# Optimization experiments

Measured on AMD Instinct MI355X. Metric: run time of the kernel, lower is better.

Reference implementation:

```python
import jax, jax.numpy as jnp
import numpy as np

HEADS = 8
DIM_HEAD = 64
SCALE = DIM_HEAD ** -0.5  # q scaling
EPS = 1e-5  # channel LayerNorm eps (float32)


def setup_inputs() -> dict:
    key = jax.random.key(0)
    ks = jax.random.split(key, 4)
    B, C, H, W = 8, 256, 64, 64
    hd = HEADS * DIM_HEAD  # 512
    x = jax.random.normal(ks[0], (B, C, H, W), dtype=jnp.float32)
    w_qkv = jax.random.normal(ks[1], (3 * hd, C), dtype=jnp.float32) * 0.02  # 1x1 conv, no bias
    w_out = jax.random.normal(ks[2], (C, hd), dtype=jnp.float32) * 0.02     # 1x1 conv
    b_out = jax.random.normal(ks[3], (C,), dtype=jnp.float32) * 0.02
    g_ln = jnp.ones((C,), dtype=jnp.float32)  # LayerNorm gamma
    return {"x": x, "w_qkv": w_qkv, "w_out": w_out, "b_out": b_out, "g_ln": g_ln}


def reference(x, w_qkv, w_out, b_out, g_ln):
    B, C, H, W = x.shape
    n = H * W
    hd = HEADS * DIM_HEAD
    # 1x1 conv == per-pixel matmul: [B,C,H,W] x [3hd,C] -> [B,3hd,H,W]
    qkv = jnp.einsum('bchw,oc->bohw', x, w_qkv).reshape(B, 3, HEADS, DIM_HEAD, n)
    q, k, v = qkv[:, 0], qkv[:, 1], qkv[:, 2]  # each [B,h,d,n]
    q = jax.nn.softmax(q, axis=-2) * SCALE      # softmax over head-dim d
    k = jax.nn.softmax(k, axis=-1)              # softmax over spatial n
    v = v / n
    context = jnp.einsum('bhdn,bhen->bhde', k, v)   # [B,h,d,e]
    out = jnp.einsum('bhde,bhdn->bhen', context, q)  # [B,h,e,n]
    out = out.reshape(B, hd, H, W)
    # to_out: 1x1 conv + bias, then channel-wise LayerNorm (gamma only)
    y = jnp.einsum('bchw,oc->bohw', out, w_out) + b_out[None, :, None, None]
    mean = jnp.mean(y, axis=1, keepdims=True)
    var = jnp.var(y, axis=1, keepdims=True)  # unbiased=False
    return (y - mean) * jax.lax.rsqrt(var + EPS) * g_ln[None, :, None, None]
```

## Files before the change

### kernel.cpp

```cpp
#include <hip/hip_runtime.h>
#include <stdint.h>


#define NB    8
#define CCH   256
#define NSP   4096
#define O3    1536
#define NH    8
#define DH    64
#define CSTR  136

typedef unsigned short u16;
typedef unsigned int   u32;
typedef __bf16 bf16;
typedef bf16  bf16x8 __attribute__((ext_vector_type(8)));
typedef float f32x4  __attribute__((ext_vector_type(4)));
typedef u16   u16x8  __attribute__((ext_vector_type(8)));
typedef u16   u16x4  __attribute__((ext_vector_type(4)));

__device__ __forceinline__ float b2f(u16 h) {
  union { u32 u; float f; } x; x.u = ((u32)h) << 16; return x.f;
}
__device__ __forceinline__ u16 f2b(float f) {
  union { float f; u32 u; } x; x.f = f;
  u32 r = x.u + 0x7fffu + ((x.u >> 16) & 1u);
  return (u16)(r >> 16);
}
__device__ __forceinline__ int detect_bf(const void* g) {
  return ((const u32*)g)[0] != 0x3F800000u;
}
__device__ __forceinline__ void ldg2lds16(const u16* g, u16* l) {
  __builtin_amdgcn_global_load_lds((const __attribute__((address_space(1))) void*)g,
                                   (__attribute__((address_space(3))) void*)l,
                                   16, 0, 0);
}

#define TSTR 68
__global__ __launch_bounds__(256) void k_prep(const void* __restrict__ xv,
                                              const void* __restrict__ wv,
                                              u16* __restrict__ xT,
                                              u16* __restrict__ Wb,
                                              float* __restrict__ S,
                                              const void* __restrict__ g_lnv) {
  const int isbf = detect_bf(g_lnv);
  const int t = threadIdx.x;
  if (blockIdx.z == 8) {
    const int tid = blockIdx.y * 64 + blockIdx.x;
    if (tid < 192) {
      const int idx = tid * 256 + t;
      const int row = idx >> 5, cu = idx & 31;
      int didx;
      if (row < 512) {
        const int h = row >> 6, i = (row >> 4) & 3, fr = row & 15;
        const int ks = cu >> 2, quad = cu & 3;
        didx = ((h * 8 + ks) * 4 + i) * 64 + quad * 16 + fr;
      } else if (row < 1024) {
        didx = (512 + ((row - 512) >> 6) * 128 + (row & 63)) * 32 + cu;
      } else {
        didx = (512 + ((row - 1024) >> 6) * 128 + 64 + (row & 63)) * 32 + cu;
      }
      if (isbf) {
        reinterpret_cast<uint4*>(Wb)[didx] = reinterpret_cast<const uint4*>(wv)[idx];
      } else {
        float4 a = reinterpret_cast<const float4*>(wv)[idx * 2];
        float4 b = reinterpret_cast<const float4*>(wv)[idx * 2 + 1];
        ushort4 o0, o1;
        o0.x = f2b(a.x); o0.y = f2b(a.y); o0.z = f2b(a.z); o0.w = f2b(a.w);
        o1.x = f2b(b.x); o1.y = f2b(b.y); o1.z = f2b(b.z); o1.w = f2b(b.w);
        reinterpret_cast<ushort4*>(Wb)[didx * 2]     = o0;
        reinterpret_cast<ushort4*>(Wb)[didx * 2 + 1] = o1;
      }
    } else if (tid < 200) {
      reinterpret_cast<float2*>(S)[(tid - 192) * 256 + t] = (float2){0.f, 0.f};
    }
    return;
  }
  const int b = blockIdx.z, cb = blockIdx.y * 64, nb = blockIdx.x * 64;
  __shared__ u16 tile[64 * TSTR];
  if (isbf) {
    const u16* xb = (const u16*)xv;
#pragma unroll
    for (int rr = 0; rr < 2; ++rr) {
      const int u = t + 256 * rr;
      const int c = u >> 3, ch = u & 7;
      u16x8 v = *reinterpret_cast<const u16x8*>(
          xb + ((size_t)(b * CCH + cb + c) * NSP + nb + ch * 8));
      u16* dst = tile + c * TSTR + ch * 8;
      *reinterpret_cast<u16x4*>(dst)     = (u16x4){v[0], v[1], v[2], v[3]};
      *reinterpret_cast<u16x4*>(dst + 4) = (u16x4){v[4], v[5], v[6], v[7]};
    }
  } else {
    const float* xb = (const float*)xv;
#pragma unroll
    for (int rr = 0; rr < 4; ++rr) {
      const int u = t + 256 * rr;
      const int c = u >> 4, c4 = u & 15;
      float4 f = *reinterpret_cast<const float4*>(
          xb + ((size_t)(b * CCH + cb + c) * NSP + nb + c4 * 4));
      u16x4 o; o[0] = f2b(f.x); o[1] = f2b(f.y); o[2] = f2b(f.z); o[3] = f2b(f.w);
      *reinterpret_cast<u16x4*>(tile + c * TSTR + c4 * 4) = o;
    }
  }
  __syncthreads();
#pragma unroll
  for (int rr = 0; rr < 2; ++rr) {
    const int u = t + 256 * rr;
    const int n = u >> 3, cc = u & 7;
    u16x8 o;
#pragma unroll
    for (int e = 0; e < 8; ++e) o[e] = tile[(cc * 8 + e) * TSTR + n];
    *reinterpret_cast<u16x8*>(
        xT + ((size_t)(b * NSP + nb + n) * CCH + cb + cc * 8)) = o;
  }
}

__global__ __launch_bounds__(256) void k_kv_mfma(const u16* __restrict__ Wb,
                                                 const u16* __restrict__ xT,
                                                 float* __restrict__ S,
                                                 float* __restrict__ ctxp) {
  __shared__ __align__(16) u16 gbuf[16384];
  __shared__ __align__(16) u16 epi[64 * CSTR * 2];
  u16* ekS = epi;
  u16* vS  = epi + 64 * CSTR;

  const int b = blockIdx.z, h = blockIdx.y, g = blockIdx.x;
  const int m0 = 512 + h * 128;
  const int t = threadIdx.x, w = t >> 6, l = t & 63;
  const int wm = (w >> 1) * 64, wn = (w & 1) * 64;
  const int fr = l & 15, quad = l >> 4;

  const u16* A = Wb;
  const u16* B = xT + (size_t)b * NSP * CCH;
  const int s0 = w * 2, s1 = s0 + 1;
  const int ra0 = s0 * 16 + (l >> 2);
  const int ra1 = s1 * 16 + (l >> 2);
  const int kc  = (l & 3) * 8;
  const int fq  = quad * 8;

  f32x4 c2[4];
#pragma unroll
  for (int j = 0; j < 4; ++j) c2[j] = (f32x4){0.f, 0.f, 0.f, 0.f};
  float sacc = 0.f;

#define STAGE_KV(SUB, KK, BUF)                                                  \
  {                                                                             \
    const int n0_ = g * 512 + (SUB) * 128;                                      \
    const int k0_ = (KK) * 32;                                                  \
    u16* As_ = gbuf + (BUF) * 8192;                                             \
    u16* Bs_ = As_ + 4096;                                                      \
    ldg2lds16(A + (size_t)(m0 + ra0) * 256 + k0_ + kc, As_ + s0 * 512);         \
    ldg2lds16(A + (size_t)(m0 + ra1) * 256 + k0_ + kc, As_ + s1 * 512);         \
    ldg2lds16(B + (size_t)(n0_ + ra0) * 256 + k0_ + kc, Bs_ + s0 * 512);        \
    ldg2lds16(B + (size_t)(n0_ + ra1) * 256 + k0_ + kc, Bs_ + s1 * 512);        \
  }

  STAGE_KV(0, 0, 0);

  for (int sub = 0; sub < 4; ++sub) {
    f32x4 acc[4][4];
#pragma unroll
    for (int i = 0; i < 4; ++i)
#pragma unroll
      for (int j = 0; j < 4; ++j) acc[i][j] = (f32x4){0.f, 0.f, 0.f, 0.f};

#pragma unroll
    for (int kk = 0; kk < 8; ++kk) {
      if (!(sub == 3 && kk == 7)) {
        const int ns = (kk < 7) ? sub : sub + 1;
        const int nk = (kk < 7) ? kk + 1 : 0;
        STAGE_KV(ns, nk, (kk + 1) & 1);
        asm volatile("s_waitcnt vmcnt(4)" ::: "memory");
      } else {
        asm volatile("s_waitcnt vmcnt(0)" ::: "memory");
      }
      __builtin_amdgcn_s_barrier();
      const u16* As = gbuf + (kk & 1) * 8192;
      const u16* Bs = As + 4096;
      bf16x8 af[4], bg[4];
#pragma unroll
      for (int i = 0; i < 4; ++i)
        af[i] = *reinterpret_cast<const bf16x8*>(As + (wm + i * 16 + fr) * 32 + fq);
#pragma unroll
      for (int j = 0; j < 4; ++j)
        bg[j] = *reinterpret_cast<const bf16x8*>(Bs + (wn + j * 16 + fr) * 32 + fq);
#pragma unroll
      for (int i = 0; i < 4; ++i)
#pragma unroll
        for (int j = 0; j < 4; ++j)
          acc[i][j] = __builtin_amdgcn_mfma_f32_16x16x32_bf16(af[i], bg[j], acc[i][j], 0, 0, 0);
      __builtin_amdgcn_s_barrier();
    }

    {
      u16* dstT = (w < 2) ? ekS : vS;
#pragma unroll
      for (int i = 0; i < 4; ++i)
#pragma unroll
        for (int r = 0; r < 4; ++r) {
          const int row = i * 16 + quad * 4 + r;
#pragma unroll
          for (int j = 0; j < 4; ++j) {
            float v = acc[i][j][r];
            if (w < 2) v = __expf(v);
            dstT[row * CSTR + wn + j * 16 + fr] = f2b(v);
          }
        }
    }
    asm volatile("s_waitcnt lgkmcnt(0)" ::: "memory");
    __builtin_amdgcn_s_barrier();

    {
      const int d = t >> 2, seg = t & 3;
      float s = 0.f;
      const u16* src = ekS + d * CSTR + seg * 32;
#pragma unroll
      for (int m = 0; m < 32; ++m) s += b2f(src[m]);
      s += __shfl_xor(s, 1);
      s += __shfl_xor(s, 2);
      sacc += s;
    }

#pragma unroll
    for (int k0 = 0; k0 < 128; k0 += 32) {
      bf16x8 af = *reinterpret_cast<const bf16x8*>(ekS + (w * 16 + fr) * CSTR + k0 + quad * 8);
#pragma unroll
      for (int j = 0; j < 4; ++j) {
        bf16x8 bg = *reinterpret_cast<const bf16x8*>(vS + (j * 16 + fr) * CSTR + k0 + quad * 8);
        c2[j] = __builtin_amdgcn_mfma_f32_16x16x32_bf16(af, bg, c2[j], 0, 0, 0);
      }
    }
  }

  float* cb = ctxp + ((size_t)g * 64 + b * NH + h) * 4096;
#pragma unroll
  for (int j = 0; j < 4; ++j)
#pragma unroll
    for (int r = 0; r < 4; ++r)
      cb[(w * 16 + quad * 4 + r) * 64 + j * 16 + fr] = c2[j][r];
  if ((t & 3) == 0) atomicAdd(&S[b * 512 + h * 64 + (t >> 2)], sacc);
#undef STAGE_KV
}

__global__ __launch_bounds__(256) void k_fold(const float* __restrict__ ctxp,
                                              const void* __restrict__ w_outv,
                                              const float* __restrict__ S,
                                              u16* __restrict__ Mb,
                                              const void* __restrict__ g_lnv) {
  const int isbf = detect_bf(g_lnv);
  const int h = blockIdx.x, b = blockIdx.y, ds = blockIdx.z * 16;
  const int t = threadIdx.x;
  __shared__ float ctxS[16][64];
  __shared__ float invS[16];
  if (t < 16) invS[t] = (1.0f / 4096.0f) / S[b * 512 + h * 64 + ds + t];
  const size_t bhoff = (size_t)(b * NH + h) * 4096 + (size_t)ds * 64;
#pragma unroll
  for (int i = 0; i < 4; ++i) {
    const int idx = t + 256 * i;
    float s = 0.f;
#pragma unroll
    for (int ch = 0; ch < 8; ++ch)
      s += ctxp[(size_t)ch * 64 * 4096 + bhoff + idx];
    ctxS[idx >> 6][idx & 63] = s;
  }
  float wrow[64];
  if (isbf) {
    const u16* wsrc = (const u16*)w_outv + (size_t)t * 512 + h * DH;
#pragma unroll
    for (int e4 = 0; e4 < 64; e4 += 4) {
      ushort4 u = *reinterpret_cast<const ushort4*>(wsrc + e4);
      wrow[e4 + 0] = b2f(u.x); wrow[e4 + 1] = b2f(u.y);
      wrow[e4 + 2] = b2f(u.z); wrow[e4 + 3] = b2f(u.w);
    }
  } else {
    const float* wsrc = (const float*)w_outv + (size_t)t * 512 + h * DH;
#pragma unroll
    for (int e4 = 0; e4 < 64; e4 += 4) {
      float4 f = *reinterpret_cast<const float4*>(wsrc + e4);
      wrow[e4 + 0] = f.x; wrow[e4 + 1] = f.y;
      wrow[e4 + 2] = f.z; wrow[e4 + 3] = f.w;
    }
  }
  __syncthreads();
  const int w_ = t >> 5, i_ = (t >> 4) & 1, fr_ = t & 15;
  const int f_ = i_ + 2 * (ds >> 5);
  const int qa = (ds & 31) >> 3;
  u16* dstF = Mb + ((((size_t)(b * 8 + w_) * 8 + h) * 4 + f_) * 64 + fr_) * 8;
  u16x8 o0, o1;
  for (int d = 0; d < 16; ++d) {
    float s = 0.f;
#pragma unroll
    for (int e = 0; e < 64; e += 4) {
      float4 c4 = *reinterpret_cast<const float4*>(&ctxS[d][e]);
      s += wrow[e] * c4.x + wrow[e + 1] * c4.y + wrow[e + 2] * c4.z + wrow[e + 3] * c4.w;
    }
    const u16 v = f2b(s * invS[d]);
    if (d < 8) o0[d] = v; else o1[d - 8] = v;
  }
  *reinterpret_cast<u16x8*>(dstF + (size_t)qa * 128)       = o0;
  *reinterpret_cast<u16x8*>(dstF + (size_t)(qa + 1) * 128) = o1;
}

__global__ __launch_bounds__(512, 4) void k_qmq_ln(const u16* __restrict__ Wb,
                                                   const u16* __restrict__ xT,
                                                   const u16* __restrict__ Mb,
                                                   const void* __restrict__ b_outv,
                                                   const void* __restrict__ g_lnv,
                                                   void* __restrict__ outv) {
  __shared__ __align__(16) u16 pool[64 * 512];
  __shared__ float redS[8][4][16];
  __shared__ float redQ[8][4][16];
  __shared__ float gS[256], bS[256];

  const int isbf = detect_bf(g_lnv);
  const int b  = blockIdx.y;
  const int n0 = blockIdx.x * 64;
  const int t  = threadIdx.x, w = t >> 6, l = t & 63;
  const int fr = l & 15, quad = l >> 4;

  if (t < 256) {
    gS[t] = isbf ? b2f(((const u16*)g_lnv)[t]) : ((const float*)g_lnv)[t];
    bS[t] = isbf ? b2f(((const u16*)b_outv)[t]) : ((const float*)b_outv)[t];
  }

  {
    const u16* Bg = xT + (size_t)b * NSP * CCH;
#pragma unroll
    for (int s = 0; s < 4; ++s) {
      const int p = w * 4 + s;
      const int r = 2 * p + (l >> 5);
      const int g16 = (l & 31) ^ (r & 7);
      ldg2lds16(Bg + (size_t)(n0 + r) * 256 + g16 * 8, pool + p * 512);
    }
    asm volatile("s_waitcnt vmcnt(0)" ::: "memory");
    __syncthreads();
  }

  f32x4 qa[4][4];
#pragma unroll
  for (int i = 0; i < 4; ++i)
#pragma unroll
    for (int j = 0; j < 4; ++j) qa[i][j] = (f32x4){0.f, 0.f, 0.f, 0.f};

  {
    const u16* AqF = Wb + (size_t)w * 16384 + (size_t)l * 8;
    bf16x8 afc[4], afn[4];
#pragma unroll
    for (int i = 0; i < 4; ++i)
      afc[i] = *reinterpret_cast<const bf16x8*>(AqF + i * 512);
#pragma unroll
    for (int ks = 0; ks < 8; ++ks) {
      if (ks < 7) {
#pragma unroll
        for (int i = 0; i < 4; ++i)
          afn[i] = *reinterpret_cast<const bf16x8*>(AqF + ((ks + 1) * 4 + i) * 512);
      }
      const int k0 = ks * 32;
      bf16x8 bg[4];
#pragma unroll
      for (int j = 0; j < 4; ++j) {
        const int row = j * 16 + fr;
        const int c16 = (k0 >> 3) + quad;
        bg[j] = *reinterpret_cast<const bf16x8*>(
            pool + row * 256 + ((c16 ^ (row & 7)) << 3));
      }
#pragma unroll
      for (int i = 0; i < 4; ++i)
#pragma unroll
        for (int j = 0; j < 4; ++j)
          qa[i][j] = __builtin_amdgcn_mfma_f32_16x16x32_bf16(afc[i], bg[j], qa[i][j], 0, 0, 0);
      if (ks < 7) {
#pragma unroll
        for (int i = 0; i < 4; ++i) afc[i] = afn[i];
      }
    }
  }
  __syncthreads();

  const u16* AmF = Mb + ((size_t)(b * 8 + w) * 16384) + (size_t)l * 8;
  bf16x8 amc[4], amn[4];
#pragma unroll
  for (int f = 0; f < 4; ++f)
    amc[f] = *reinterpret_cast<const bf16x8*>(AmF + f * 512);

#pragma unroll
  for (int j = 0; j < 4; ++j) {
    float s = 0.f;
#pragma unroll
    for (int i = 0; i < 4; ++i)
#pragma unroll
      for (int r = 0; r < 4; ++r) { qa[i][j][r] = __expf(qa[i][j][r]); s += qa[i][j][r]; }
    s += __shfl_xor(s, 16);
    s += __shfl_xor(s, 32);
    const float inv = 0.125f / s;
    const int n   = j * 16 + fr;
    const int swz = (n & 7) << 4;
#pragma unroll
    for (int i = 0; i < 4; ++i) {
      ushort4 o;
      o.x = f2b(qa[i][j][0] * inv); o.y = f2b(qa[i][j][1] * inv);
      o.z = f2b(qa[i][j][2] * inv); o.w = f2b(qa[i][j][3] * inv);
      const int hd2 = (w * 64 + i * 16 + quad * 4) * 2;
      *reinterpret_cast<ushort4*>(
          reinterpret_cast<char*>(pool) + ((n * 1024 + hd2) ^ swz)) = o;
    }
  }
  __syncthreads();

  f32x4 acc[2][4];
#pragma unroll
  for (int i = 0; i < 2; ++i)
#pragma unroll
    for (int j = 0; j < 4; ++j) acc[i][j] = (f32x4){0.f, 0.f, 0.f, 0.f};

  {
#pragma unroll
    for (int kt = 0; kt < 8; ++kt) {
      if (kt < 7) {
#pragma unroll
        for (int f = 0; f < 4; ++f)
          amn[f] = *reinterpret_cast<const bf16x8*>(AmF + ((kt + 1) * 4 + f) * 512);
      }
      const int k0 = kt * 64;
      bf16x8 bg0[4], bg1[4];
#pragma unroll
      for (int j = 0; j < 4; ++j) {
        const int n = j * 16 + fr;
        const int o0 = (n * 1024 + k0 * 2 + quad * 16) ^ ((n & 7) << 4);
        const int o1 = (n * 1024 + (k0 + 32) * 2 + quad * 16) ^ ((n & 7) << 4);
        bg0[j] = *reinterpret_cast<const bf16x8*>(reinterpret_cast<const char*>(pool) + o0);
        bg1[j] = *reinterpret_cast<const bf16x8*>(reinterpret_cast<const char*>(pool) + o1);
      }
#pragma unroll
      for (int i = 0; i < 2; ++i)
#pragma unroll
        for (int j = 0; j < 4; ++j)
          acc[i][j] = __builtin_amdgcn_mfma_f32_16x16x32_bf16(amc[i], bg0[j], acc[i][j], 0, 0, 0);
#pragma unroll
      for (int i = 0; i < 2; ++i)
#pragma unroll
        for (int j = 0; j < 4; ++j)
          acc[i][j] = __builtin_amdgcn_mfma_f32_16x16x32_bf16(amc[i + 2], bg1[j], acc[i][j], 0, 0, 0);
      if (kt < 7) {
#pragma unroll
        for (int f = 0; f < 4; ++f) amc[f] = amn[f];
      }
    }
  }

  float ps[4] = {}, pq[4] = {};
#pragma unroll
  for (int i = 0; i < 2; ++i)
#pragma unroll
    for (int r = 0; r < 4; ++r) {
      const int c = w * 32 + i * 16 + quad * 4 + r;
      const float bi = bS[c];
#pragma unroll
      for (int j = 0; j < 4; ++j) {
        acc[i][j][r] += bi;
        ps[j] += acc[i][j][r];
        pq[j] += acc[i][j][r] * acc[i][j][r];
      }
    }
#pragma unroll
  for (int j = 0; j < 4; ++j) {
    ps[j] += __shfl_xor(ps[j], 16); ps[j] += __shfl_xor(ps[j], 32);
    pq[j] += __shfl_xor(pq[j], 16); pq[j] += __shfl_xor(pq[j], 32);
  }
  if (quad == 0) {
#pragma unroll
    for (int j = 0; j < 4; ++j) { redS[w][j][fr] = ps[j]; redQ[w][j][fr] = pq[j]; }
  }
  __syncthreads();
  float mean[4], inv[4];
#pragma unroll
  for (int j = 0; j < 4; ++j) {
    float s = 0.f, q = 0.f;
#pragma unroll
    for (int g = 0; g < 8; ++g) { s += redS[g][j][fr]; q += redQ[g][j][fr]; }
    const float mn = s * (1.0f / 256.0f);
    const float vr = q * (1.0f / 256.0f) - mn * mn;
    mean[j] = mn;
    inv[j] = rsqrtf(vr + 1e-5f);
  }

#pragma unroll
  for (int i = 0; i < 2; ++i)
#pragma unroll
    for (int r = 0; r < 4; ++r) {
      const int c = w * 32 + i * 16 + quad * 4 + r;
      const float g = gS[c];
#pragma unroll
      for (int j = 0; j < 4; ++j) {
        const int col = n0 + j * 16 + fr;
        const float o = (acc[i][j][r] - mean[j]) * inv[j] * g;
        const size_t idx = ((size_t)b * CCH + c) * NSP + col;
        if (isbf) ((u16*)outv)[idx] = f2b(o);
        else      ((float*)outv)[idx] = o;
      }
    }
}

extern "C" void kernel_launch(void* const* d_in, const int* in_sizes, int n_in,
                              void* d_out, int out_size, void* d_ws, size_t ws_size,
                              hipStream_t stream) {
  (void)in_sizes; (void)n_in; (void)out_size; (void)ws_size;
  const void* x     = d_in[0];
  const void* w_qkv = d_in[1];
  const void* w_out = d_in[2];
  const void* b_out = d_in[3];
  const void* g_ln  = d_in[4];

  char* ws = (char*)d_ws;
  u16*   Wb   = (u16*)(ws + 256);
  float* S    = (float*)(ws + 851968);
  u16*   xT   = (u16*)(ws + 1048576);
  float* ctxp = (float*)(ws + 17825792);
  u16*   Mb   = (u16*)(ws + 26214400);

  k_prep    <<<dim3(64, 4, 9),  256, 0, stream>>>(x, w_qkv, xT, Wb, S, g_ln);
  k_kv_mfma <<<dim3(8, NH, NB), 256, 0, stream>>>(Wb, xT, S, ctxp);
  k_fold    <<<dim3(NH, NB, 4), 256, 0, stream>>>(ctxp, w_out, S, Mb, g_ln);
  k_qmq_ln  <<<dim3(64, NB),    512, 0, stream>>>(Wb, xT, Mb, b_out, g_ln, d_out);
}
```

Measured before the change: 161.8 us.

## Load K/V weights directly from pre-swizzled global layout into registers

The prep kernel now stores the K/V rows of the QKV weight in an MFMA-fragment-ordered layout, so the kv kernel reads A fragments straight from global memory into registers, prefetching one k-step ahead, instead of staging them through LDS. Only the x tile goes through LDS now, which halves the shared buffer and the per-step async loads. An XOR swizzle is applied to the B tile writes and reads to reduce LDS bank conflicts. The cost is extra VGPRs for the double-buffered A fragments and reliance on L2 hits for repeated weight reads.

```diff
diff --git a/kernel.cpp b/kernel.cpp
--- a/kernel.cpp
+++ b/kernel.cpp
@@ -49,15 +49,17 @@
     if (tid < 192) {
       const int idx = tid * 256 + t;
       const int row = idx >> 5, cu = idx & 31;
+      const int ks = cu >> 2, qd = cu & 3;
       int didx;
       if (row < 512) {
         const int h = row >> 6, i = (row >> 4) & 3, fr = row & 15;
-        const int ks = cu >> 2, quad = cu & 3;
-        didx = ((h * 8 + ks) * 4 + i) * 64 + quad * 16 + fr;
-      } else if (row < 1024) {
-        didx = (512 + ((row - 512) >> 6) * 128 + (row & 63)) * 32 + cu;
+        didx = ((h * 8 + ks) * 4 + i) * 64 + qd * 16 + fr;
       } else {
-        didx = (512 + ((row - 1024) >> 6) * 128 + 64 + (row & 63)) * 32 + cu;
+        int h, mrow;
+        if (row < 1024) { h = (row - 512) >> 6;  mrow = row & 63; }
+        else            { h = (row - 1024) >> 6; mrow = 64 + (row & 63); }
+        const int mh = mrow >> 6, i = (mrow >> 4) & 3, fr = mrow & 15;
+        didx = 16384 + (((h * 2 + mh) * 8 + ks) * 4 + i) * 64 + qd * 16 + fr;
       }
       if (isbf) {
         reinterpret_cast<uint4*>(Wb)[didx] = reinterpret_cast<const uint4*>(wv)[idx];
@@ -118,43 +120,43 @@
                                                  const u16* __restrict__ xT,
                                                  float* __restrict__ S,
                                                  float* __restrict__ ctxp) {
-  __shared__ __align__(16) u16 gbuf[16384];
+  __shared__ __align__(16) u16 gbuf[8192];
   __shared__ __align__(16) u16 epi[64 * CSTR * 2];
   u16* ekS = epi;
   u16* vS  = epi + 64 * CSTR;
 
   const int b = blockIdx.z, h = blockIdx.y, g = blockIdx.x;
-  const int m0 = 512 + h * 128;
   const int t = threadIdx.x, w = t >> 6, l = t & 63;
-  const int wm = (w >> 1) * 64, wn = (w & 1) * 64;
+  const int wn = (w & 1) * 64;
   const int fr = l & 15, quad = l >> 4;
 
-  const u16* A = Wb;
   const u16* B = xT + (size_t)b * NSP * CCH;
   const int s0 = w * 2, s1 = s0 + 1;
   const int ra0 = s0 * 16 + (l >> 2);
   const int ra1 = s1 * 16 + (l >> 2);
-  const int kc  = (l & 3) * 8;
-  const int fq  = quad * 8;
+  const int kcs = ((l & 3) ^ ((l >> 3) & 3)) * 8;
+  const int fsw = (quad ^ ((fr >> 1) & 3)) * 8;
+  const u16* AkF = Wb + 131072 + (size_t)(h * 2 + (w >> 1)) * 16384 + (size_t)l * 8;
 
   f32x4 c2[4];
 #pragma unroll
   for (int j = 0; j < 4; ++j) c2[j] = (f32x4){0.f, 0.f, 0.f, 0.f};
   float sacc = 0.f;
 
-#define STAGE_KV(SUB, KK, BUF)                                                  \
+#define STAGE_B(SUB, KK, BUF)                                                   \
   {                                                                             \
     const int n0_ = g * 512 + (SUB) * 128;                                      \
     const int k0_ = (KK) * 32;                                                  \
-    u16* As_ = gbuf + (BUF) * 8192;                                             \
-    u16* Bs_ = As_ + 4096;                                                      \
-    ldg2lds16(A + (size_t)(m0 + ra0) * 256 + k0_ + kc, As_ + s0 * 512);         \
-    ldg2lds16(A + (size_t)(m0 + ra1) * 256 + k0_ + kc, As_ + s1 * 512);         \
-    ldg2lds16(B + (size_t)(n0_ + ra0) * 256 + k0_ + kc, Bs_ + s0 * 512);        \
-    ldg2lds16(B + (size_t)(n0_ + ra1) * 256 + k0_ + kc, Bs_ + s1 * 512);        \
-  }
-
-  STAGE_KV(0, 0, 0);
+    u16* Bs_ = gbuf + (BUF) * 4096;                                             \
+    ldg2lds16(B + (size_t)(n0_ + ra0) * 256 + k0_ + kcs, Bs_ + s0 * 512);       \
+    ldg2lds16(B + (size_t)(n0_ + ra1) * 256 + k0_ + kcs, Bs_ + s1 * 512);       \
+  }
+
+  STAGE_B(0, 0, 0);
+  bf16x8 afc[4], afn[4];
+#pragma unroll
+  for (int i = 0; i < 4; ++i)
+    afc[i] = *reinterpret_cast<const bf16x8*>(AkF + i * 512);
 
   for (int sub = 0; sub < 4; ++sub) {
     f32x4 acc[4][4];
@@ -165,30 +167,36 @@
 
 #pragma unroll
     for (int kk = 0; kk < 8; ++kk) {
-      if (!(sub == 3 && kk == 7)) {
+      const bool last = (sub == 3 && kk == 7);
+      const int nk = (kk < 7) ? kk + 1 : 0;
+      if (!last) {
         const int ns = (kk < 7) ? sub : sub + 1;
-        const int nk = (kk < 7) ? kk + 1 : 0;
-        STAGE_KV(ns, nk, (kk + 1) & 1);
-        asm volatile("s_waitcnt vmcnt(4)" ::: "memory");
+        STAGE_B(ns, nk, (kk + 1) & 1);
+        asm volatile("s_waitcnt vmcnt(2)" ::: "memory");
       } else {
         asm volatile("s_waitcnt vmcnt(0)" ::: "memory");
       }
       __builtin_amdgcn_s_barrier();
-      const u16* As = gbuf + (kk & 1) * 8192;
-      const u16* Bs = As + 4096;
-      bf16x8 af[4], bg[4];
+      if (!last) {
+#pragma unroll
+        for (int i = 0; i < 4; ++i)
+          afn[i] = *reinterpret_cast<const bf16x8*>(AkF + (nk * 4 + i) * 512);
+      }
+      const u16* Bs = gbuf + (kk & 1) * 4096;
+      bf16x8 bg[4];
+#pragma unroll
+      for (int j = 0; j < 4; ++j)
+        bg[j] = *reinterpret_cast<const bf16x8*>(Bs + (wn + j * 16 + fr) * 32 + fsw);
 #pragma unroll
       for (int i = 0; i < 4; ++i)
-        af[i] = *reinterpret_cast<const bf16x8*>(As + (wm + i * 16 + fr) * 32 + fq);
-#pragma unroll
-      for (int j = 0; j < 4; ++j)
-        bg[j] = *reinterpret_cast<const bf16x8*>(Bs + (wn + j * 16 + fr) * 32 + fq);
-#pragma unroll
-      for (int i = 0; i < 4; ++i)
 #pragma unroll
         for (int j = 0; j < 4; ++j)
-          acc[i][j] = __builtin_amdgcn_mfma_f32_16x16x32_bf16(af[i], bg[j], acc[i][j], 0, 0, 0);
+          acc[i][j] = __builtin_amdgcn_mfma_f32_16x16x32_bf16(afc[i], bg[j], acc[i][j], 0, 0, 0);
       __builtin_amdgcn_s_barrier();
+      if (!last) {
+#pragma unroll
+        for (int i = 0; i < 4; ++i) afc[i] = afn[i];
+      }
     }
 
     {
@@ -238,7 +246,7 @@
     for (int r = 0; r < 4; ++r)
       cb[(w * 16 + quad * 4 + r) * 64 + j * 16 + fr] = c2[j][r];
   if ((t & 3) == 0) atomicAdd(&S[b * 512 + h * 64 + (t >> 2)], sacc);
-#undef STAGE_KV
+#undef STAGE_B
 }
 
 __global__ __launch_bounds__(256) void k_fold(const float* __restrict__ ctxp,
```

Result: no change. 161.0 us (-0.5%).
